# Kernel optimization log

Measured on AMD Instinct MI355X. Metric: run time of the kernel, lower is better.

Reference implementation:

```python
import jax, jax.numpy as jnp
import numpy as np

B, LQ, LK, D, H = 8, 512, 512, 512, 128

def setup_inputs() -> dict:
    key = jax.random.key(0)
    k1, k2, k3, k4, k5 = jax.random.split(key, 5)
    qs = jax.random.normal(k1, (B, LQ, D), dtype=jnp.float32)
    ks = jax.random.normal(k2, (B, LK, D), dtype=jnp.float32)
    # Dense kernels: flax Dense stores kernel as [in_features, out_features]
    Wq = jax.random.normal(k3, (D, H), dtype=jnp.float32) / np.sqrt(D)
    Wk = jax.random.normal(k4, (D, H), dtype=jnp.float32) / np.sqrt(D)
    wv = jax.random.normal(k5, (H,), dtype=jnp.float32) / np.sqrt(H)
    return {"qs": qs, "ks": ks, "Wq": Wq, "Wk": Wk, "wv": wv}

def reference(qs, ks, Wq, Wk, wv):
    # Project queries and keys into the shared hidden space: [B,Lq,H], [B,Lk,H]
    q = jnp.einsum("bqd,dh->bqh", qs, Wq)
    k = jnp.einsum("bkd,dh->bkh", ks, Wk)
    # Broadcast-add -> tanh -> linear reduce over H: scores [B,Lq,Lk]
    feats = jnp.tanh(q[:, :, None, :] + k[:, None, :, :])  # [B,Lq,Lk,H]
    return jnp.einsum("bqkh,h->bqk", feats, wv)
```

## Files before the change

### kernel.cpp

```cpp
#include <hip/hip_runtime.h>
#include <hip/hip_bf16.h>
#include <cstdint>

#define B_   8
#define LQ_  512
#define LK_  512
#define D_   512
#define H_   128

typedef __attribute__((ext_vector_type(8))) short  short8;
typedef __attribute__((ext_vector_type(4))) float  float4v;

#define TANH_C 2.8853900817779268f

__device__ __forceinline__ short bf16rne(float x) {
  uint32_t u = __float_as_uint(x);
  return (short)((u + 0x7fffu + ((u >> 16) & 1u)) >> 16);
}

__global__ __launch_bounds__(256) void prep_kernel(
    const float* __restrict__ Wq, const float* __restrict__ Wk,
    const float* __restrict__ wv,
    short* __restrict__ WqF, short* __restrict__ WkF,
    float* __restrict__ w2, float* __restrict__ W0buf) {
  int g = blockIdx.x * 256 + threadIdx.x;
  if (blockIdx.x == 0) {
    int t = threadIdx.x;
    if (t < H_) w2[t] = -2.0f * wv[t];
    if (t == H_) {
      float s = 0.f;
      for (int h = 0; h < H_; ++h) s += wv[h];
      W0buf[0] = s;
    }
  }
  int m = g >> 13;
  int r = g & 8191;
  int l  = r & 63;
  int kb = (r >> 6) & 15;
  int nt = r >> 10;
  int col = nt * 16 + (l & 15);
  int k0  = kb * 32 + ((l >> 4) << 3);
  const float* W = m ? Wk : Wq;
  short8 f;
#pragma unroll
  for (int j = 0; j < 8; ++j) f[j] = bf16rne(W[(k0 + j) * H_ + col]);
  ((short8*)(m ? WkF : WqF))[r] = f;
}

__global__ __launch_bounds__(256) void proj_kernel(
    const float* __restrict__ qs, const float* __restrict__ ks,
    const short* __restrict__ WqF, const short* __restrict__ WkF,
    float* __restrict__ qp, float* __restrict__ kp) {
  int blk  = blockIdx.x;
  int wave = threadIdx.x >> 6;
  int l    = threadIdx.x & 63;
  int grow = blk * 16;
  int m    = (grow >= 4096) ? 1 : 0;
  int r0   = grow - (m ? 4096 : 0);
  const float*  A  = m ? ks : qs;
  const short8* BF = (const short8*)(m ? WkF : WqF);
  float* out = m ? kp : qp;

  float4v acc[2];
  acc[0] = (float4v){0.f, 0.f, 0.f, 0.f};
  acc[1] = (float4v){0.f, 0.f, 0.f, 0.f};

  int quad = l >> 4;
  int arow = r0 + (l & 15);
  const float* aptr = A + (size_t)arow * D_ + quad * 8;
  int t0 = wave * 2;

#pragma unroll 4
  for (int kb = 0; kb < 16; ++kb) {
    float4v a0 = *(const float4v*)(aptr + kb * 32);
    float4v a1 = *(const float4v*)(aptr + kb * 32 + 4);
    short8 af;
#pragma unroll
    for (int j = 0; j < 4; ++j) { af[j] = bf16rne(a0[j]); af[j + 4] = bf16rne(a1[j]); }
#pragma unroll
    for (int tt = 0; tt < 2; ++tt) {
      short8 bf = BF[((t0 + tt) * 16 + kb) * 64 + l];
      acc[tt] = __builtin_amdgcn_mfma_f32_16x16x32_bf16(af, bf, acc[tt], 0, 0, 0);
    }
  }

#pragma unroll
  for (int tt = 0; tt < 2; ++tt)
#pragma unroll
    for (int r = 0; r < 4; ++r) {
      int row = r0 + quad * 4 + r;
      int col = (t0 + tt) * 16 + (l & 15);
      out[(size_t)row * H_ + col] = __builtin_amdgcn_exp2f(acc[tt][r] * TANH_C);
    }
}

__global__ __launch_bounds__(128, 2) void score_kernel(
    const float* __restrict__ qp, const float* __restrict__ kp,
    const float* __restrict__ w2, const float* __restrict__ W0buf,
    float* __restrict__ out) {
  __shared__ float qt[64 * 68];
  __shared__ float kt[32 * 68];
  __shared__ float wl[H_];

  int b = blockIdx.z, qtile = blockIdx.y, ktile = blockIdx.x;
  int t = threadIdx.x;
  int tx = t & 7, ty = t >> 3;

  const float* qbase = qp + (size_t)(b * LQ_ + qtile * 64) * H_;
  const float* kbase = kp + (size_t)(b * LK_ + ktile * 32) * H_;

  float W0 = W0buf[0];

  if (t < 32) *(float4v*)&wl[t * 4] = *(const float4v*)&w2[t * 4];

  float4v acc4[4][4];
  const float4v ones = (float4v){1.f, 1.f, 1.f, 1.f};
#pragma unroll
  for (int i = 0; i < 4; ++i)
#pragma unroll
    for (int j = 0; j < 4; ++j) acc4[i][j] = (float4v){0.f, 0.f, 0.f, 0.f};

  int lr = t >> 4, lc = t & 15;

  for (int hc = 0; hc < 2; ++hc) {
    __syncthreads();
#pragma unroll
    for (int s = 0; s < 8; ++s) {
      int row = lr + 8 * s;
      *(float4v*)&qt[row * 68 + lc * 4] =
          *(const float4v*)&qbase[row * H_ + hc * 64 + lc * 4];
    }
#pragma unroll
    for (int s = 0; s < 4; ++s) {
      int row = lr + 8 * s;
      *(float4v*)&kt[row * 68 + lc * 4] =
          *(const float4v*)&kbase[row * H_ + hc * 64 + lc * 4];
    }
    __syncthreads();

#pragma unroll 4
    for (int h0 = 0; h0 < 64; h0 += 4) {
      float4v qv[4], kv[4];
#pragma unroll
      for (int i = 0; i < 4; ++i) qv[i] = *(const float4v*)&qt[(ty + 16 * i) * 68 + h0];
#pragma unroll
      for (int j = 0; j < 4; ++j) kv[j] = *(const float4v*)&kt[(tx + 8 * j) * 68 + h0];
      float4v w4 = *(const float4v*)&wl[hc * 64 + h0];

#pragma unroll
      for (int i = 0; i < 4; ++i)
#pragma unroll
        for (int j = 0; j < 4; ++j) {
          float4v den = __builtin_elementwise_fma(qv[i], kv[j], ones);
          float4v r;
          r[0] = __builtin_amdgcn_rcpf(den[0]);
          r[1] = __builtin_amdgcn_rcpf(den[1]);
          r[2] = __builtin_amdgcn_rcpf(den[2]);
          r[3] = __builtin_amdgcn_rcpf(den[3]);
          acc4[i][j] = __builtin_elementwise_fma(w4, r, acc4[i][j]);
        }
    }
  }

  size_t ob = (size_t)(b * LQ_ + qtile * 64) * LK_ + ktile * 32;
#pragma unroll
  for (int i = 0; i < 4; ++i)
#pragma unroll
    for (int j = 0; j < 4; ++j) {
      float4v a = acc4[i][j];
      out[ob + (size_t)(ty + 16 * i) * LK_ + tx + 8 * j] =
          W0 + ((a[0] + a[1]) + (a[2] + a[3]));
    }
}

extern "C" void kernel_launch(void* const* d_in, const int* in_sizes, int n_in,
                              void* d_out, int out_size, void* d_ws, size_t ws_size,
                              hipStream_t stream) {
  const float* qs = (const float*)d_in[0];
  const float* ks = (const float*)d_in[1];
  const float* Wq = (const float*)d_in[2];
  const float* Wk = (const float*)d_in[3];
  const float* wv = (const float*)d_in[4];
  float* out = (float*)d_out;

  char* ws = (char*)d_ws;
  short* WqF  = (short*)ws;
  short* WkF  = (short*)(ws + (128 << 10));
  float* qp   = (float*)(ws + (256 << 10));
  float* kp   = (float*)(ws + (256 << 10) + (2 << 20));
  float* w2   = (float*)(ws + (256 << 10) + (4 << 20));
  float* W0b  = (float*)(ws + (256 << 10) + (4 << 20) + 512);

  prep_kernel<<<64, 256, 0, stream>>>(Wq, Wk, wv, WqF, WkF, w2, W0b);
  proj_kernel<<<512, 256, 0, stream>>>(qs, ks, WqF, WkF, qp, kp);
  score_kernel<<<dim3(16, 8, 8), 128, 0, stream>>>(qp, kp, w2, W0b, out);
}
```

Baseline: 112.3 us.

## Combine four reciprocals into one via common denominator in score kernel

Rewrites the tanh-sum inner loop so four h terms share a single reciprocal: the products of denominators and a combined numerator are formed with FMAs, then one rcp is taken per group of four. To make this vectorize, the k tile is stored transposed in shared memory, so each thread holds four consecutive k columns per h and writes its outputs as float4. This reduces transcendental rcp instructions fourfold in exchange for extra multiplies. It risks overflow or precision loss when the product of four exp-scaled denominators grows very large.

```diff
diff --git a/kernel.cpp b/kernel.cpp
--- a/kernel.cpp
+++ b/kernel.cpp
@@ -16,6 +16,10 @@
 __device__ __forceinline__ short bf16rne(float x) {
   uint32_t u = __float_as_uint(x);
   return (short)((u + 0x7fffu + ((u >> 16) & 1u)) >> 16);
+}
+
+__device__ __forceinline__ float4v splat4(float x) {
+  return (float4v){x, x, x, x};
 }
 
 __global__ __launch_bounds__(256) void prep_kernel(
@@ -99,7 +103,7 @@
     const float* __restrict__ w2, const float* __restrict__ W0buf,
     float* __restrict__ out) {
   __shared__ float qt[64 * 68];
-  __shared__ float kt[32 * 68];
+  __shared__ float kt[64 * 36];
   __shared__ float wl[H_];
 
   int b = blockIdx.z, qtile = blockIdx.y, ktile = blockIdx.x;
@@ -113,12 +117,10 @@
 
   if (t < 32) *(float4v*)&wl[t * 4] = *(const float4v*)&w2[t * 4];
 
-  float4v acc4[4][4];
+  float4v acc[4];
   const float4v ones = (float4v){1.f, 1.f, 1.f, 1.f};
 #pragma unroll
-  for (int i = 0; i < 4; ++i)
-#pragma unroll
-    for (int j = 0; j < 4; ++j) acc4[i][j] = (float4v){0.f, 0.f, 0.f, 0.f};
+  for (int i = 0; i < 4; ++i) acc[i] = (float4v){0.f, 0.f, 0.f, 0.f};
 
   int lr = t >> 4, lc = t & 15;
 
@@ -133,44 +135,49 @@
 #pragma unroll
     for (int s = 0; s < 4; ++s) {
       int row = lr + 8 * s;
-      *(float4v*)&kt[row * 68 + lc * 4] =
-          *(const float4v*)&kbase[row * H_ + hc * 64 + lc * 4];
+      float4v g = *(const float4v*)&kbase[row * H_ + hc * 64 + lc * 4];
+#pragma unroll
+      for (int u = 0; u < 4; ++u) kt[(lc * 4 + u) * 36 + row] = g[u];
     }
     __syncthreads();
 
 #pragma unroll 4
     for (int h0 = 0; h0 < 64; h0 += 4) {
-      float4v qv[4], kv[4];
-#pragma unroll
-      for (int i = 0; i < 4; ++i) qv[i] = *(const float4v*)&qt[(ty + 16 * i) * 68 + h0];
-#pragma unroll
-      for (int j = 0; j < 4; ++j) kv[j] = *(const float4v*)&kt[(tx + 8 * j) * 68 + h0];
+      float4v kv[4];
+#pragma unroll
+      for (int hh = 0; hh < 4; ++hh)
+        kv[hh] = *(const float4v*)&kt[(h0 + hh) * 36 + tx * 4];
       float4v w4 = *(const float4v*)&wl[hc * 64 + h0];
 
 #pragma unroll
-      for (int i = 0; i < 4; ++i)
-#pragma unroll
-        for (int j = 0; j < 4; ++j) {
-          float4v den = __builtin_elementwise_fma(qv[i], kv[j], ones);
-          float4v r;
-          r[0] = __builtin_amdgcn_rcpf(den[0]);
-          r[1] = __builtin_amdgcn_rcpf(den[1]);
-          r[2] = __builtin_amdgcn_rcpf(den[2]);
-          r[3] = __builtin_amdgcn_rcpf(den[3]);
-          acc4[i][j] = __builtin_elementwise_fma(w4, r, acc4[i][j]);
-        }
+      for (int i = 0; i < 4; ++i) {
+        float4v qv = *(const float4v*)&qt[(ty + 16 * i) * 68 + h0];
+        float4v den0 = __builtin_elementwise_fma(splat4(qv[0]), kv[0], ones);
+        float4v den1 = __builtin_elementwise_fma(splat4(qv[1]), kv[1], ones);
+        float4v den2 = __builtin_elementwise_fma(splat4(qv[2]), kv[2], ones);
+        float4v den3 = __builtin_elementwise_fma(splat4(qv[3]), kv[3], ones);
+        float4v d01 = den0 * den1;
+        float4v d23 = den2 * den3;
+        float4v P   = d01 * d23;
+        float4v n01 = __builtin_elementwise_fma(splat4(w4[1]), den0, splat4(w4[0]) * den1);
+        float4v n23 = __builtin_elementwise_fma(splat4(w4[3]), den2, splat4(w4[2]) * den3);
+        float4v N   = __builtin_elementwise_fma(n01, d23, n23 * d01);
+        float4v r;
+        r[0] = __builtin_amdgcn_rcpf(P[0]);
+        r[1] = __builtin_amdgcn_rcpf(P[1]);
+        r[2] = __builtin_amdgcn_rcpf(P[2]);
+        r[3] = __builtin_amdgcn_rcpf(P[3]);
+        acc[i] = __builtin_elementwise_fma(N, r, acc[i]);
+      }
     }
   }
 
   size_t ob = (size_t)(b * LQ_ + qtile * 64) * LK_ + ktile * 32;
 #pragma unroll
-  for (int i = 0; i < 4; ++i)
-#pragma unroll
-    for (int j = 0; j < 4; ++j) {
-      float4v a = acc4[i][j];
-      out[ob + (size_t)(ty + 16 * i) * LK_ + tx + 8 * j] =
-          W0 + ((a[0] + a[1]) + (a[2] + a[3]));
-    }
+  for (int i = 0; i < 4; ++i) {
+    float4v o = acc[i] + splat4(W0);
+    *(float4v*)&out[ob + (size_t)(ty + 16 * i) * LK_ + tx * 4] = o;
+  }
 }
 
 extern "C" void kernel_launch(void* const* d_in, const int* in_sizes, int n_in,
```

After: 110.6 us. No clear change (-1.5%).
